# Performance work log

Hardware: AMD Instinct MI355X
Metric: run time of the kernel (lower is better)

Reference implementation:

```python
import jax, jax.numpy as jnp
import numpy as np

B, D_IN, D_H = 4096, 1024, 1024  # cell_dim == hidden_dim required by the elementwise math


def _lin(x, W, b):
    # torch nn.Linear: y = x @ W.T + b, W: [out, in]
    return x @ W.T + b


def setup_inputs() -> dict:
    key = jax.random.key(0)
    ks = jax.random.split(key, 20)
    s2 = 1.0 / np.sqrt(D_IN + D_H)
    s1 = 1.0 / np.sqrt(D_IN)
    inp = {
        "input_tensor": jax.random.normal(ks[0], (B, D_IN), jnp.float32),
        "h_cur": jax.random.uniform(ks[1], (B, D_H), jnp.float32),
        "excited_cell": jax.random.uniform(ks[2], (B, D_H), jnp.float32),
        "time_cell": jax.random.uniform(ks[3], (B, D_H), jnp.float32),
        "Wt_w": jax.random.normal(ks[4], (D_H, D_IN + D_H), jnp.float32) * s2,
        "Wt_b": jax.random.normal(ks[5], (D_H,), jnp.float32) * s2,
        "Wa_w": jax.random.normal(ks[6], (D_H, D_IN + D_H), jnp.float32) * s2,
        "Wa_b": jax.random.normal(ks[7], (D_H,), jnp.float32) * s2,
        "Eh_w": jax.random.normal(ks[8], (D_H, D_IN + D_H), jnp.float32) * s2,
        "Eh_b": jax.random.normal(ks[9], (D_H,), jnp.float32) * s2,
        "Hw_w": jax.random.normal(ks[10], (D_H, D_IN + D_H), jnp.float32) * s2,
        "Hw_b": jax.random.normal(ks[11], (D_H,), jnp.float32) * s2,
        "Tr_w": jax.random.normal(ks[12], (D_H, D_IN), jnp.float32) * s1,
        "Tr_b": jax.random.normal(ks[13], (D_H,), jnp.float32) * s1,
        "Ei_w": jax.random.normal(ks[14], (D_H, D_IN), jnp.float32) * s1,
        "Ei_b": jax.random.normal(ks[15], (D_H,), jnp.float32) * s1,
    }
    return inp


def reference(input_tensor, h_cur, excited_cell, time_cell,
              Wt_w, Wt_b, Wa_w, Wa_b, Eh_w, Eh_b, Hw_w, Hw_b,
              Tr_w, Tr_b, Ei_w, Ei_b):
    combined = jnp.concatenate([input_tensor, h_cur], axis=1)  # [B, D_IN+D_H]
    energy_init = jax.nn.sigmoid(_lin(input_tensor, Ei_w, Ei_b))
    ratio = jax.nn.sigmoid(_lin(input_tensor, Tr_w, Tr_b))
    up_time = jnp.tanh(_lin(combined, Wt_w, Wt_b))
    time_cell = ratio * jax.nn.relu(time_cell + up_time) - 1.0
    leap = (time_cell <= 0).astype(jnp.float32)
    time_cell = (1.0 - leap) * time_cell
    energy = leap * excited_cell
    excited_cell = excited_cell - energy + energy_init * (1.0 - leap)
    absorb_energy = jax.nn.sigmoid(_lin(combined, Wa_w, Wa_b))
    excited_cell = excited_cell + absorb_energy
    h_up = h_cur * energy
    h_state = jnp.tanh(_lin(jnp.concatenate([input_tensor, h_up], axis=1), Eh_w, Eh_b))
    h_weight = jax.nn.sigmoid(_lin(combined, Hw_w, Hw_b))
    h_next = jnp.tanh((1.0 - h_weight) * h_cur + h_weight * h_state)
    return (h_next, excited_cell, time_cell)
```

## Files before the change

### kernel.cpp

```cpp
#include <hip/hip_runtime.h>
#include <math.h>


typedef __attribute__((ext_vector_type(4))) float f32x4;
typedef __attribute__((ext_vector_type(8))) _Float16 half8;
typedef __attribute__((ext_vector_type(4))) _Float16 half4;

#define NEL (4096 * 1024)
#define DELTA 3.0e-3f
#define COLCAP 256

__device__ __forceinline__ float sigm(float x) { return 1.0f / (1.0f + expf(-x)); }

__device__ __forceinline__ void gload16(const void* g, void* l) {
  __builtin_amdgcn_global_load_lds(
      (const __attribute__((address_space(1))) void*)g,
      (__attribute__((address_space(3))) void*)l, 16, 0, 0);
}

template <int OP, int NT>
__device__ void gemm256(_Float16* sm, const int brow, const int bcol,
                        const _Float16* A1, const _Float16* A2,
                        const _Float16* W, const float* bias,
                        float* outF, _Float16* outH)
{
  const int tid = threadIdx.x;
  const int lane = tid & 63, w = tid >> 6;
  const int wr = w >> 2, wc = w & 3;
  const int lr = lane & 15, lq = lane >> 4;

  const int s0 = tid, s1 = tid + 512;
  const int r0 = ((s0 >> 5) << 3) | (s0 & 7), c0 = (s0 >> 3) & 3;
  const int r1 = ((s1 >> 5) << 3) | (s1 & 7), c1 = (s1 >> 3) & 3;

  int pA[8], pB[4];
#pragma unroll
  for (int m = 0; m < 8; ++m) {
    const int R = wr * 128 + m * 16 + lr;
    pA[m] = ((((R >> 3) << 5) | (R & 7)) | (lq << 3)) * 8;
  }
#pragma unroll
  for (int n = 0; n < 4; ++n) {
    const int R = wc * 64 + n * 16 + lr;
    pB[n] = ((((R >> 3) << 5) | (R & 7)) | (lq << 3)) * 8;
  }

  auto issue = [&](int tt, int g, int bfx) {
    _Float16* dst = sm + bfx * 32768 + g * 8192;
    const int kh = g >> 1;
    if ((g & 1) == 0) {
      const _Float16* Ap = (NT == 32 && tt >= 16) ? A2 : A1;
      const int kk = ((NT == 32) ? (tt & 15) : tt) * 64 + kh * 32;
      gload16(Ap + (size_t)(brow + r0) * 1024 + kk + c0 * 8, dst + s0 * 8);
      gload16(Ap + (size_t)(brow + r1) * 1024 + kk + c1 * 8, dst + s1 * 8);
    } else {
      const int kk = tt * 64 + kh * 32;
      gload16(W + (size_t)(bcol + r0) * (NT * 64) + kk + c0 * 8, dst + s0 * 8);
      gload16(W + (size_t)(bcol + r1) * (NT * 64) + kk + c1 * 8, dst + s1 * 8);
    }
  };

  f32x4 acc[8][4] = {};

  asm volatile("s_waitcnt vmcnt(0)" ::: "memory");
  __builtin_amdgcn_sched_barrier(0);

  issue(0, 0, 0); issue(0, 1, 0); issue(0, 2, 0); issue(0, 3, 0);

#define QPHASE(KH, CH, GRP)                                                   \
  {                                                                           \
    if (more) issue(t + 1, GRP, nx);                                          \
    const _Float16* Ab = sm + bf * 32768 + (KH) * 16384;                      \
    const _Float16* Bb = Ab + 8192;                                           \
    half8 a_[4], b_[4];                                                       \
    _Pragma("unroll") for (int mm = 0; mm < 4; ++mm)                          \
        a_[mm] = *(const half8*)(Ab + pA[(CH) * 4 + mm]);                     \
    _Pragma("unroll") for (int nn = 0; nn < 4; ++nn)                          \
        b_[nn] = *(const half8*)(Bb + pB[nn]);                                \
    __builtin_amdgcn_s_setprio(1);                                            \
    _Pragma("unroll") for (int mm = 0; mm < 4; ++mm)                          \
        _Pragma("unroll") for (int nn = 0; nn < 4; ++nn)                      \
            acc[(CH) * 4 + mm][nn] = __builtin_amdgcn_mfma_f32_16x16x32_f16(  \
                a_[mm], b_[nn], acc[(CH) * 4 + mm][nn], 0, 0, 0);             \
    __builtin_amdgcn_s_setprio(0);                                            \
  }

  for (int t = 0; t < NT; ++t) {
    const int bf = t & 1, nx = bf ^ 1;
    const bool more = (t + 1) < NT;
    asm volatile("s_waitcnt vmcnt(4)" ::: "memory");
    __builtin_amdgcn_s_barrier();
    QPHASE(0, 0, 0)
    __builtin_amdgcn_s_barrier();
    QPHASE(0, 1, 1)
    if (more) { asm volatile("s_waitcnt vmcnt(4)" ::: "memory"); }
    else      { asm volatile("s_waitcnt vmcnt(0)" ::: "memory"); }
    __builtin_amdgcn_s_barrier();
    QPHASE(1, 0, 2)
    __builtin_amdgcn_s_barrier();
    QPHASE(1, 1, 3)
  }
#undef QPHASE

  __builtin_amdgcn_sched_barrier(0);
  float bv[4];
#pragma unroll
  for (int n = 0; n < 4; ++n) bv[n] = bias[bcol + wc * 64 + n * 16 + lr];
#pragma unroll
  for (int m = 0; m < 8; ++m)
#pragma unroll
    for (int n = 0; n < 4; ++n) {
      const int col = bcol + wc * 64 + n * 16 + lr;
#pragma unroll
      for (int j = 0; j < 4; ++j) {
        const int row = brow + wr * 128 + m * 16 + lq * 4 + j;
        const size_t idx = (size_t)row * 1024 + col;
        const float v = acc[m][n][j] + bv[n];
        if (OP == 0)      outF[idx] = sigm(v);
        else if (OP == 1) outF[idx] = tanhf(v);
        else              outH[idx] = (_Float16)sigm(v);
      }
    }
}

__global__ __launch_bounds__(512, 2)
void qurnn_gemm256(const _Float16* inpH, const _Float16* hcH,
                   const _Float16* WtH, const float* Wt_b,
                   const _Float16* WaH, const float* Wa_b,
                   const _Float16* HwH, const float* Hw_b,
                   const _Float16* TrH, const float* Tr_b,
                   const _Float16* EiH, const float* Ei_b,
                   float* ws_ut, _Float16* ws_ab, _Float16* ws_hw,
                   float* out_tm, _Float16* ws_ei)
{
  __shared__ __align__(16) _Float16 sm[65536];
  const int b = blockIdx.x;
  const int tile = (b < 192) ? (b & 63) : (b - 192);
  const int brow = (tile & 15) * 256;
  const int bcol = (tile >> 4) * 256;
  if (b < 64) {
    gemm256<1, 32>(sm, brow, bcol, inpH, hcH, WtH, Wt_b, ws_ut, nullptr);
  } else if (b < 128) {
    gemm256<2, 32>(sm, brow, bcol, inpH, hcH, WaH, Wa_b, nullptr, ws_ab);
  } else if (b < 192) {
    gemm256<2, 32>(sm, brow, bcol, inpH, hcH, HwH, Hw_b, nullptr, ws_hw);
  } else {
    gemm256<0, 16>(sm, brow, bcol, inpH, nullptr, TrH, Tr_b, out_tm, nullptr);
    gemm256<2, 16>(sm, brow, bcol, inpH, nullptr, EiH, Ei_b, nullptr, ws_ei);
  }
}

template <int OP>
__device__ __forceinline__ void gemm_body(
    _Float16* sm, const int brow, const int bcol,
    const _Float16* A1h, const _Float16* A2h,
    const _Float16* Wh, const float* bias, const int K,
    float* outF, _Float16* outH, const _Float16* hw_p, const float* hc_p)
{
  _Float16* As = sm;
  _Float16* Bs = sm + 8192;
  const int tid = threadIdx.x;
  const int lane = tid & 63;
  const int w = tid >> 6;
  const int wr = w >> 1, wc = w & 1;
  const int lr = lane & 15, lq = lane >> 4;

  f32x4 acc[4][4] = {};

  for (int k0 = 0; k0 < K; k0 += 64) {
    const _Float16* Ah = (k0 < 1024) ? A1h : A2h;
    const int kk = k0 & 1023;
    __syncthreads();
#pragma unroll
    for (int i = 0; i < 4; ++i) {
      const int c_lin = i * 256 + tid;
      const int row = c_lin >> 3;
      const int c = c_lin & 7;
      const int src = (c ^ (row & 7)) * 8;
      gload16(Ah + (size_t)(brow + row) * 1024 + kk + src, &As[row * 64 + c * 8]);
      gload16(Wh + (size_t)(bcol + row) * K + k0 + src,    &Bs[row * 64 + c * 8]);
    }
    __syncthreads();

#pragma unroll
    for (int h = 0; h < 2; ++h) {
      half8 a[4], b[4];
#pragma unroll
      for (int m = 0; m < 4; ++m) {
        const int row = wr * 64 + m * 16 + lr;
        const int ch = (lq + 4 * h) ^ (row & 7);
        a[m] = *(const half8*)&As[row * 64 + ch * 8];
      }
#pragma unroll
      for (int n = 0; n < 4; ++n) {
        const int row = wc * 64 + n * 16 + lr;
        const int ch = (lq + 4 * h) ^ (row & 7);
        b[n] = *(const half8*)&Bs[row * 64 + ch * 8];
      }
#pragma unroll
      for (int m = 0; m < 4; ++m)
#pragma unroll
        for (int n = 0; n < 4; ++n)
          acc[m][n] = __builtin_amdgcn_mfma_f32_16x16x32_f16(a[m], b[n], acc[m][n], 0, 0, 0);
    }
  }

  float bv[4];
#pragma unroll
  for (int n = 0; n < 4; ++n) bv[n] = bias[bcol + wc * 64 + n * 16 + lr];

#pragma unroll
  for (int m = 0; m < 4; ++m)
#pragma unroll
    for (int n = 0; n < 4; ++n) {
      const int col = bcol + wc * 64 + n * 16 + lr;
#pragma unroll
      for (int j = 0; j < 4; ++j) {
        const int rowg = brow + wr * 64 + m * 16 + lq * 4 + j;
        const size_t idx = (size_t)rowg * 1024 + col;
        const float v = acc[m][n][j] + bv[n];
        if (OP == 3) {
          const float hs = tanhf(v);
          const float hwv = (float)hw_p[idx];
          const float hcv = hc_p[idx];
          outF[idx] = tanhf((1.0f - hwv) * hcv + hwv * hs);
        }
      }
    }
}

__global__ __launch_bounds__(256, 3)
void qurnn_eh(const _Float16* inpH, const _Float16* hup,
              const _Float16* EhH, const float* Eh_b,
              const _Float16* hw, const float* hcur, float* out_h)
{
  __shared__ __align__(16) _Float16 sm[2 * 8192];
  const int brow = (blockIdx.x & 31) * 128;
  const int bcol = (blockIdx.x >> 5) * 128;
  gemm_body<3>(sm, brow, bcol, inpH, hup, EhH, Eh_b, 2048,
               out_h, nullptr, hw, hcur);
}

__global__ __launch_bounds__(256)
void qurnn_cell(const f32x4* tc, const f32x4* ec, const f32x4* hc,
                const f32x4* ut, const half4* ab, const half4* ei,
                f32x4* out_ex, f32x4* out_tm, half4* hup,
                int* colcnt, int* collist)
{
  const int i = blockIdx.x * 256 + threadIdx.x;
  const f32x4 tcv = tc[i], ecv = ec[i], hcv = hc[i];
  const f32x4 rav = out_tm[i];
  const f32x4 utv = ut[i];
  const half4 abv = ab[i], eiv = ei[i];
  f32x4 to, eo; half4 ho;
#pragma unroll
  for (int j = 0; j < 4; ++j) {
    const float t = rav[j] * fmaxf(tcv[j] + utv[j], 0.0f) - 1.0f;
    const bool leap = (t <= 0.0f);
    to[j] = leap ? 0.0f : t;
    eo[j] = (leap ? 0.0f : ecv[j] + (float)eiv[j]) + (float)abv[j];
    ho[j] = (_Float16)(leap ? hcv[j] * ecv[j] : 0.0f);
    if (fabsf(t) < DELTA) {
      const int e = i * 4 + j;
      const int col = e & 1023;
      const int p = atomicAdd(&colcnt[col], 1);
      if (p < COLCAP) collist[col * COLCAP + p] = e >> 10;
    }
  }
  out_tm[i] = to;
  out_ex[i] = eo;
  hup[i] = ho;
}

__global__ __launch_bounds__(256)
void qurnn_fixup(const int* colcnt, const int* collist,
                 const float* inp, const float* hcur,
                 const float* Tr_w, const float* Tr_b,
                 const float* Wt_w, const float* Wt_b,
                 const _Float16* ei, const _Float16* ab,
                 const float* tc, const float* ec,
                 float* out_tm, float* out_ex, _Float16* hup)
{
  const int col = blockIdx.x;
  const int n_c = min(colcnt[col], COLCAP);
  if (n_c == 0) return;
  __shared__ float wTr[1024];
  __shared__ float wWt[2048];
  const int tid = threadIdx.x;
  for (int k = tid; k < 1024; k += 256) wTr[k] = Tr_w[(size_t)col * 1024 + k];
  for (int k = tid; k < 2048; k += 256) wWt[k] = Wt_w[(size_t)col * 2048 + k];
  __syncthreads();

  const int wid = tid >> 6, lane = tid & 63;
  for (int e = wid; e < n_c; e += 4) {
    const int row = collist[col * COLCAP + e];
    const int idx = row * 1024 + col;
    const f32x4* irow = (const f32x4*)(inp  + (size_t)row * 1024);
    const f32x4* hrow = (const f32x4*)(hcur + (size_t)row * 1024);
    float dTr = 0.0f, dWt = 0.0f;
#pragma unroll
    for (int k = 0; k < 4; ++k) {
      const int q = k * 64 + lane;
      const f32x4 a = irow[q], h = hrow[q];
      const f32x4 w1 = *(const f32x4*)&wTr[q * 4];
      const f32x4 w2 = *(const f32x4*)&wWt[q * 4];
      const f32x4 w3 = *(const f32x4*)&wWt[1024 + q * 4];
#pragma unroll
      for (int j = 0; j < 4; ++j) {
        dTr = fmaf(a[j], w1[j], dTr);
        dWt = fmaf(a[j], w2[j], dWt);
        dWt = fmaf(h[j], w3[j], dWt);
      }
    }
#pragma unroll
    for (int s = 32; s; s >>= 1) {
      dTr += __shfl_xor(dTr, s);
      dWt += __shfl_xor(dWt, s);
    }
    if (lane == 0) {
      const float ratio = sigm(dTr + Tr_b[col]);
      const float utv = tanhf(dWt + Wt_b[col]);
      const float t = ratio * fmaxf(tc[idx] + utv, 0.0f) - 1.0f;
      const bool leap = (t <= 0.0f);
      out_tm[idx] = leap ? 0.0f : t;
      out_ex[idx] = (leap ? 0.0f : ec[idx] + (float)ei[idx]) + (float)ab[idx];
      hup[idx] = (_Float16)(leap ? hcur[idx] * ec[idx] : 0.0f);
    }
  }
}

__global__ __launch_bounds__(256)
void convert_k(const float* inp, const float* hcur,
               const float* Wt_w, const float* Tr_w, const float* Wa_w,
               const float* Hw_w, const float* Eh_w, const float* Ei_w,
               _Float16* inpH, _Float16* hcH, _Float16* WtH, _Float16* TrH,
               _Float16* WaH, _Float16* HwH, _Float16* EhH, _Float16* EiH,
               int* colcnt)
{
  if (blockIdx.z == 0 && blockIdx.x == 0) {
    for (int k = threadIdx.x; k < 1024; k += 256) colcnt[k] = 0;
  }
  const float* src; _Float16* dh; int n4;
  switch (blockIdx.z) {
    case 0: src = inp;  dh = inpH; n4 = NEL / 4;           break;
    case 1: src = hcur; dh = hcH;  n4 = NEL / 4;           break;
    case 2: src = Wt_w; dh = WtH;  n4 = (1024 * 2048) / 4; break;
    case 3: src = Tr_w; dh = TrH;  n4 = (1024 * 1024) / 4; break;
    case 4: src = Wa_w; dh = WaH;  n4 = (1024 * 2048) / 4; break;
    case 5: src = Hw_w; dh = HwH;  n4 = (1024 * 2048) / 4; break;
    case 6: src = Eh_w; dh = EhH;  n4 = (1024 * 2048) / 4; break;
    default:src = Ei_w; dh = EiH;  n4 = (1024 * 1024) / 4; break;
  }
  for (int i = blockIdx.x * 256 + threadIdx.x; i < n4; i += gridDim.x * 256) {
    const f32x4 v = ((const f32x4*)src)[i];
    half4 h;
#pragma unroll
    for (int j = 0; j < 4; ++j) h[j] = (_Float16)v[j];
    ((half4*)dh)[i] = h;
  }
}

extern "C" void kernel_launch(void* const* d_in, const int* in_sizes, int n_in,
                              void* d_out, int out_size, void* d_ws, size_t ws_size,
                              hipStream_t stream)
{
  const float* inp  = (const float*)d_in[0];
  const float* hcur = (const float*)d_in[1];
  const float* ec   = (const float*)d_in[2];
  const float* tc   = (const float*)d_in[3];
  const float* Wt_w = (const float*)d_in[4];
  const float* Wt_b = (const float*)d_in[5];
  const float* Wa_w = (const float*)d_in[6];
  const float* Wa_b = (const float*)d_in[7];
  const float* Eh_w = (const float*)d_in[8];
  const float* Eh_b = (const float*)d_in[9];
  const float* Hw_w = (const float*)d_in[10];
  const float* Hw_b = (const float*)d_in[11];
  const float* Tr_w = (const float*)d_in[12];
  const float* Tr_b = (const float*)d_in[13];
  const float* Ei_w = (const float*)d_in[14];
  const float* Ei_b = (const float*)d_in[15];

  float* out_h  = (float*)d_out;
  float* out_ex = out_h + NEL;
  float* out_tm = out_ex + NEL;

  char* wsb = (char*)d_ws;
  float*    ws_ut  = (float*)(wsb);
  _Float16* ws_ab  = (_Float16*)(wsb + (16u << 20));
  _Float16* ws_ei  = (_Float16*)(wsb + (24u << 20));
  _Float16* ws_hup = (_Float16*)(wsb + (32u << 20));
  _Float16* ws_hw  = (_Float16*)(wsb + (40u << 20));
  _Float16* inpH   = (_Float16*)(wsb + (48u << 20));
  _Float16* hcH    = (_Float16*)(wsb + (56u << 20));
  _Float16* WtH    = (_Float16*)(wsb + (64u << 20));
  _Float16* TrH    = (_Float16*)(wsb + (68u << 20));
  _Float16* WaH    = (_Float16*)(wsb + (70u << 20));
  _Float16* HwH    = (_Float16*)(wsb + (74u << 20));
  _Float16* EhH    = (_Float16*)(wsb + (78u << 20));
  _Float16* EiH    = (_Float16*)(wsb + (82u << 20));
  int*      d_ccnt = (int*)(wsb + (84u << 20));
  int*      d_clst = (int*)(wsb + (84u << 20) + 4096);

  convert_k<<<dim3(512, 1, 8), 256, 0, stream>>>(
      inp, hcur, Wt_w, Tr_w, Wa_w, Hw_w, Eh_w, Ei_w,
      inpH, hcH, WtH, TrH, WaH, HwH, EhH, EiH, d_ccnt);

  qurnn_gemm256<<<dim3(256), 512, 0, stream>>>(
      inpH, hcH, WtH, Wt_b, WaH, Wa_b, HwH, Hw_b, TrH, Tr_b, EiH, Ei_b,
      ws_ut, ws_ab, ws_hw, out_tm, ws_ei);

  qurnn_cell<<<dim3(4096), 256, 0, stream>>>(
      (const f32x4*)tc, (const f32x4*)ec, (const f32x4*)hcur,
      (const f32x4*)ws_ut, (const half4*)ws_ab, (const half4*)ws_ei,
      (f32x4*)out_ex, (f32x4*)out_tm, (half4*)ws_hup, d_ccnt, d_clst);

  qurnn_fixup<<<dim3(1024), 256, 0, stream>>>(
      d_ccnt, d_clst, inp, hcur, Tr_w, Tr_b, Wt_w, Wt_b,
      ws_ei, ws_ab, tc, ec, out_tm, out_ex, ws_hup);

  qurnn_eh<<<dim3(256), 256, 0, stream>>>(
      inpH, ws_hup, EhH, Eh_b, ws_hw, hcur, out_h);
}
```

Before: 218.3 us.

## Rework GEMM main loop scheduling and store up_time and ratio intermediates in fp16

```diff
diff --git a/kernel.cpp b/kernel.cpp
--- a/kernel.cpp
+++ b/kernel.cpp
@@ -7,8 +7,8 @@
 typedef __attribute__((ext_vector_type(4))) _Float16 half4;
 
 #define NEL (4096 * 1024)
-#define DELTA 3.0e-3f
-#define COLCAP 256
+#define DELTA 4.0e-3f
+#define COLCAP 512
 
 __device__ __forceinline__ float sigm(float x) { return 1.0f / (1.0f + expf(-x)); }
 
@@ -18,11 +18,12 @@
       (__attribute__((address_space(3))) void*)l, 16, 0, 0);
 }
 
+#define SB() __builtin_amdgcn_sched_barrier(0)
+
 template <int OP, int NT>
 __device__ void gemm256(_Float16* sm, const int brow, const int bcol,
                         const _Float16* A1, const _Float16* A2,
-                        const _Float16* W, const float* bias,
-                        float* outF, _Float16* outH)
+                        const _Float16* W, const float* bias, _Float16* outH)
 {
   const int tid = threadIdx.x;
   const int lane = tid & 63, w = tid >> 6;
@@ -63,46 +64,82 @@
   f32x4 acc[8][4] = {};
 
   asm volatile("s_waitcnt vmcnt(0)" ::: "memory");
-  __builtin_amdgcn_sched_barrier(0);
-
+  SB();
   issue(0, 0, 0); issue(0, 1, 0); issue(0, 2, 0); issue(0, 3, 0);
-
-#define QPHASE(KH, CH, GRP)                                                   \
-  {                                                                           \
-    if (more) issue(t + 1, GRP, nx);                                          \
-    const _Float16* Ab = sm + bf * 32768 + (KH) * 16384;                      \
-    const _Float16* Bb = Ab + 8192;                                           \
-    half8 a_[4], b_[4];                                                       \
-    _Pragma("unroll") for (int mm = 0; mm < 4; ++mm)                          \
-        a_[mm] = *(const half8*)(Ab + pA[(CH) * 4 + mm]);                     \
-    _Pragma("unroll") for (int nn = 0; nn < 4; ++nn)                          \
-        b_[nn] = *(const half8*)(Bb + pB[nn]);                                \
-    __builtin_amdgcn_s_setprio(1);                                            \
-    _Pragma("unroll") for (int mm = 0; mm < 4; ++mm)                          \
-        _Pragma("unroll") for (int nn = 0; nn < 4; ++nn)                      \
-            acc[(CH) * 4 + mm][nn] = __builtin_amdgcn_mfma_f32_16x16x32_f16(  \
-                a_[mm], b_[nn], acc[(CH) * 4 + mm][nn], 0, 0, 0);             \
-    __builtin_amdgcn_s_setprio(0);                                            \
-  }
+  asm volatile("s_waitcnt vmcnt(4)" ::: "memory");
+  SB();
+  __builtin_amdgcn_s_barrier();
+  SB();
 
   for (int t = 0; t < NT; ++t) {
     const int bf = t & 1, nx = bf ^ 1;
     const bool more = (t + 1) < NT;
-    asm volatile("s_waitcnt vmcnt(4)" ::: "memory");
-    __builtin_amdgcn_s_barrier();
-    QPHASE(0, 0, 0)
-    __builtin_amdgcn_s_barrier();
-    QPHASE(0, 1, 1)
+    const _Float16* Ab0 = sm + bf * 32768;
+    const _Float16* Bb0 = Ab0 + 8192;
+    const _Float16* Ab1 = Ab0 + 16384;
+    const _Float16* Bb1 = Ab0 + 24576;
+    half8 a_[4], b_[4];
+
+#pragma unroll
+    for (int n = 0; n < 4; ++n) b_[n] = *(const half8*)(Bb0 + pB[n]);
+#pragma unroll
+    for (int m = 0; m < 4; ++m) a_[m] = *(const half8*)(Ab0 + pA[m]);
+    if (more) issue(t + 1, 0, nx);
+    SB(); __builtin_amdgcn_s_barrier(); SB();
+    __builtin_amdgcn_s_setprio(1);
+#pragma unroll
+    for (int m = 0; m < 4; ++m)
+#pragma unroll
+      for (int n = 0; n < 4; ++n)
+        acc[m][n] = __builtin_amdgcn_mfma_f32_16x16x32_f16(a_[m], b_[n], acc[m][n], 0, 0, 0);
+    __builtin_amdgcn_s_setprio(0);
+    SB(); __builtin_amdgcn_s_barrier(); SB();
+
+#pragma unroll
+    for (int m = 0; m < 4; ++m) a_[m] = *(const half8*)(Ab0 + pA[4 + m]);
+    if (more) issue(t + 1, 1, nx);
+    SB(); __builtin_amdgcn_s_barrier(); SB();
+    __builtin_amdgcn_s_setprio(1);
+#pragma unroll
+    for (int m = 0; m < 4; ++m)
+#pragma unroll
+      for (int n = 0; n < 4; ++n)
+        acc[4 + m][n] = __builtin_amdgcn_mfma_f32_16x16x32_f16(a_[m], b_[n], acc[4 + m][n], 0, 0, 0);
+    __builtin_amdgcn_s_setprio(0);
     if (more) { asm volatile("s_waitcnt vmcnt(4)" ::: "memory"); }
     else      { asm volatile("s_waitcnt vmcnt(0)" ::: "memory"); }
-    __builtin_amdgcn_s_barrier();
-    QPHASE(1, 0, 2)
-    __builtin_amdgcn_s_barrier();
-    QPHASE(1, 1, 3)
-  }
-#undef QPHASE
-
-  __builtin_amdgcn_sched_barrier(0);
+    SB(); __builtin_amdgcn_s_barrier(); SB();
+
+#pragma unroll
+    for (int n = 0; n < 4; ++n) b_[n] = *(const half8*)(Bb1 + pB[n]);
+#pragma unroll
+    for (int m = 0; m < 4; ++m) a_[m] = *(const half8*)(Ab1 + pA[m]);
+    if (more) issue(t + 1, 2, nx);
+    SB(); __builtin_amdgcn_s_barrier(); SB();
+    __builtin_amdgcn_s_setprio(1);
+#pragma unroll
+    for (int m = 0; m < 4; ++m)
+#pragma unroll
+      for (int n = 0; n < 4; ++n)
+        acc[m][n] = __builtin_amdgcn_mfma_f32_16x16x32_f16(a_[m], b_[n], acc[m][n], 0, 0, 0);
+    __builtin_amdgcn_s_setprio(0);
+    SB(); __builtin_amdgcn_s_barrier(); SB();
+
+#pragma unroll
+    for (int m = 0; m < 4; ++m) a_[m] = *(const half8*)(Ab1 + pA[4 + m]);
+    if (more) issue(t + 1, 3, nx);
+    SB(); __builtin_amdgcn_s_barrier(); SB();
+    __builtin_amdgcn_s_setprio(1);
+#pragma unroll
+    for (int m = 0; m < 4; ++m)
+#pragma unroll
+      for (int n = 0; n < 4; ++n)
+        acc[4 + m][n] = __builtin_amdgcn_mfma_f32_16x16x32_f16(a_[m], b_[n], acc[4 + m][n], 0, 0, 0);
+    __builtin_amdgcn_s_setprio(0);
+    if (more) { asm volatile("s_waitcnt vmcnt(4)" ::: "memory"); }
+    SB(); __builtin_amdgcn_s_barrier(); SB();
+  }
+
   float bv[4];
 #pragma unroll
   for (int n = 0; n < 4; ++n) bv[n] = bias[bcol + wc * 64 + n * 16 + lr];
@@ -116,9 +153,7 @@
         const int row = brow + wr * 128 + m * 16 + lq * 4 + j;
         const size_t idx = (size_t)row * 1024 + col;
         const float v = acc[m][n][j] + bv[n];
-        if (OP == 0)      outF[idx] = sigm(v);
-        else if (OP == 1) outF[idx] = tanhf(v);
-        else              outH[idx] = (_Float16)sigm(v);
+        outH[idx] = (_Float16)(OP == 1 ? tanhf(v) : sigm(v));
       }
     }
 }
@@ -130,8 +165,8 @@
                    const _Float16* HwH, const float* Hw_b,
                    const _Float16* TrH, const float* Tr_b,
                    const _Float16* EiH, const float* Ei_b,
-                   float* ws_ut, _Float16* ws_ab, _Float16* ws_hw,
-                   float* out_tm, _Float16* ws_ei)
+                   _Float16* ws_ut, _Float16* ws_ab, _Float16* ws_hw,
+                   _Float16* ws_ra, _Float16* ws_ei)
 {
   __shared__ __align__(16) _Float16 sm[65536];
   const int b = blockIdx.x;
@@ -139,26 +174,28 @@
   const int brow = (tile & 15) * 256;
   const int bcol = (tile >> 4) * 256;
   if (b < 64) {
-    gemm256<1, 32>(sm, brow, bcol, inpH, hcH, WtH, Wt_b, ws_ut, nullptr);
+    gemm256<1, 32>(sm, brow, bcol, inpH, hcH, WtH, Wt_b, ws_ut);
   } else if (b < 128) {
-    gemm256<2, 32>(sm, brow, bcol, inpH, hcH, WaH, Wa_b, nullptr, ws_ab);
+    gemm256<2, 32>(sm, brow, bcol, inpH, hcH, WaH, Wa_b, ws_ab);
   } else if (b < 192) {
-    gemm256<2, 32>(sm, brow, bcol, inpH, hcH, HwH, Hw_b, nullptr, ws_hw);
+    gemm256<2, 32>(sm, brow, bcol, inpH, hcH, HwH, Hw_b, ws_hw);
   } else {
-    gemm256<0, 16>(sm, brow, bcol, inpH, nullptr, TrH, Tr_b, out_tm, nullptr);
-    gemm256<2, 16>(sm, brow, bcol, inpH, nullptr, EiH, Ei_b, nullptr, ws_ei);
-  }
-}
-
-template <int OP>
-__device__ __forceinline__ void gemm_body(
-    _Float16* sm, const int brow, const int bcol,
-    const _Float16* A1h, const _Float16* A2h,
-    const _Float16* Wh, const float* bias, const int K,
-    float* outF, _Float16* outH, const _Float16* hw_p, const float* hc_p)
-{
+    gemm256<2, 16>(sm, brow, bcol, inpH, nullptr, TrH, Tr_b, ws_ra);
+    __syncthreads();
+    gemm256<2, 16>(sm, brow, bcol, inpH, nullptr, EiH, Ei_b, ws_ei);
+  }
+}
+
+__global__ __launch_bounds__(256, 3)
+void qurnn_eh(const _Float16* inpH, const _Float16* hup,
+              const _Float16* EhH, const float* Eh_b,
+              const _Float16* hw, const float* hcur, float* out_h)
+{
+  __shared__ __align__(16) _Float16 sm[2 * 8192];
   _Float16* As = sm;
   _Float16* Bs = sm + 8192;
+  const int brow = (blockIdx.x & 31) * 128;
+  const int bcol = (blockIdx.x >> 5) * 128;
   const int tid = threadIdx.x;
   const int lane = tid & 63;
   const int w = tid >> 6;
@@ -167,8 +204,8 @@
 
   f32x4 acc[4][4] = {};
 
-  for (int k0 = 0; k0 < K; k0 += 64) {
-    const _Float16* Ah = (k0 < 1024) ? A1h : A2h;
+  for (int k0 = 0; k0 < 2048; k0 += 64) {
+    const _Float16* Ah = (k0 < 1024) ? inpH : hup;
     const int kk = k0 & 1023;
     __syncthreads();
 #pragma unroll
@@ -178,7 +215,7 @@
       const int c = c_lin & 7;
       const int src = (c ^ (row & 7)) * 8;
       gload16(Ah + (size_t)(brow + row) * 1024 + kk + src, &As[row * 64 + c * 8]);
-      gload16(Wh + (size_t)(bcol + row) * K + k0 + src,    &Bs[row * 64 + c * 8]);
+      gload16(EhH + (size_t)(bcol + row) * 2048 + k0 + src, &Bs[row * 64 + c * 8]);
     }
     __syncthreads();
 
@@ -207,7 +244,7 @@
 
   float bv[4];
 #pragma unroll
-  for (int n = 0; n < 4; ++n) bv[n] = bias[bcol + wc * 64 + n * 16 + lr];
+  for (int n = 0; n < 4; ++n) bv[n] = Eh_b[bcol + wc * 64 + n * 16 + lr];
 
 #pragma unroll
   for (int m = 0; m < 4; ++m)
@@ -218,44 +255,27 @@
       for (int j = 0; j < 4; ++j) {
         const int rowg = brow + wr * 64 + m * 16 + lq * 4 + j;
         const size_t idx = (size_t)rowg * 1024 + col;
-        const float v = acc[m][n][j] + bv[n];
-        if (OP == 3) {
-          const float hs = tanhf(v);
-          const float hwv = (float)hw_p[idx];
-          const float hcv = hc_p[idx];
-          outF[idx] = tanhf((1.0f - hwv) * hcv + hwv * hs);
-        }
+        const float hs = tanhf(acc[m][n][j] + bv[n]);
+        const float hwv = (float)hw[idx];
+        const float hcv = hcur[idx];
+        out_h[idx] = tanhf((1.0f - hwv) * hcv + hwv * hs);
       }
     }
-}
-
-__global__ __launch_bounds__(256, 3)
-void qurnn_eh(const _Float16* inpH, const _Float16* hup,
-              const _Float16* EhH, const float* Eh_b,
-              const _Float16* hw, const float* hcur, float* out_h)
-{
-  __shared__ __align__(16) _Float16 sm[2 * 8192];
-  const int brow = (blockIdx.x & 31) * 128;
-  const int bcol = (blockIdx.x >> 5) * 128;
-  gemm_body<3>(sm, brow, bcol, inpH, hup, EhH, Eh_b, 2048,
-               out_h, nullptr, hw, hcur);
 }
 
 __global__ __launch_bounds__(256)
 void qurnn_cell(const f32x4* tc, const f32x4* ec, const f32x4* hc,
-                const f32x4* ut, const half4* ab, const half4* ei,
-                f32x4* out_ex, f32x4* out_tm, half4* hup,
+                const half4* ut, const half4* ra, const half4* ab,
+                const half4* ei, f32x4* out_ex, f32x4* out_tm, half4* hup,
                 int* colcnt, int* collist)
 {
   const int i = blockIdx.x * 256 + threadIdx.x;
   const f32x4 tcv = tc[i], ecv = ec[i], hcv = hc[i];
-  const f32x4 rav = out_tm[i];
-  const f32x4 utv = ut[i];
-  const half4 abv = ab[i], eiv = ei[i];
+  const half4 utv = ut[i], rav = ra[i], abv = ab[i], eiv = ei[i];
   f32x4 to, eo; half4 ho;
 #pragma unroll
   for (int j = 0; j < 4; ++j) {
-    const float t = rav[j] * fmaxf(tcv[j] + utv[j], 0.0f) - 1.0f;
+    const float t = (float)rav[j] * fmaxf(tcv[j] + (float)utv[j], 0.0f) - 1.0f;
     const bool leap = (t <= 0.0f);
     to[j] = leap ? 0.0f : t;
     eo[j] = (leap ? 0.0f : ecv[j] + (float)eiv[j]) + (float)abv[j];
@@ -386,7 +406,8 @@
   float* out_tm = out_ex + NEL;
 
   char* wsb = (char*)d_ws;
-  float*    ws_ut  = (float*)(wsb);
+  _Float16* ws_ut  = (_Float16*)(wsb);
+  _Float16* ws_ra  = (_Float16*)(wsb + (8u  << 20));
   _Float16* ws_ab  = (_Float16*)(wsb + (16u << 20));
   _Float16* ws_ei  = (_Float16*)(wsb + (24u << 20));
   _Float16* ws_hup = (_Float16*)(wsb + (32u << 20));
@@ -408,12 +429,13 @@
 
   qurnn_gemm256<<<dim3(256), 512, 0, stream>>>(
       inpH, hcH, WtH, Wt_b, WaH, Wa_b, HwH, Hw_b, TrH, Tr_b, EiH, Ei_b,
-      ws_ut, ws_ab, ws_hw, out_tm, ws_ei);
+      ws_ut, ws_ab, ws_hw, ws_ra, ws_ei);
 
   qurnn_cell<<<dim3(4096), 256, 0, stream>>>(
       (const f32x4*)tc, (const f32x4*)ec, (const f32x4*)hcur,
-      (const f32x4*)ws_ut, (const half4*)ws_ab, (const half4*)ws_ei,
-      (f32x4*)out_ex, (f32x4*)out_tm, (half4*)ws_hup, d_ccnt, d_clst);
+      (const half4*)ws_ut, (const half4*)ws_ra, (const half4*)ws_ab,
+      (const half4*)ws_ei, (f32x4*)out_ex, (f32x4*)out_tm, (half4*)ws_hup,
+      d_ccnt, d_clst);
 
   qurnn_fixup<<<dim3(1024), 256, 0, stream>>>(
       d_ccnt, d_clst, inp, hcur, Tr_w, Tr_b, Wt_w, Wt_b,
```

Result: slower. 234.1 us (+7.2%).
